# Optimization experiments

Hardware: AMD Instinct MI355X
Metric: run time of the kernel (lower is better)

The kernel has to match this reference:

```python
import jax, jax.numpy as jnp
import numpy as np


def setup_inputs() -> dict:
    key = jax.random.key(0)
    k1, k2 = jax.random.split(key)
    B, C, H, W = 4, 64, 256, 256
    x = jax.random.normal(k1, (B, C, H, W), dtype=jnp.float32)
    perspective = jax.random.uniform(k2, (B, 1, H, W), dtype=jnp.float32)
    alpha = jnp.ones((1,), dtype=jnp.float32) * 3.0   # sigma scale
    beta = jnp.ones((1,), dtype=jnp.float32)          # sigmoid slope
    gamma = jnp.zeros((1,), dtype=jnp.float32)        # sigmoid shift
    return {"x": x, "perspective": perspective, "alpha": alpha,
            "beta": beta, "gamma": gamma, "kernel_size": 7}


def reference(x, perspective, alpha, beta, gamma, kernel_size):
    K = int(kernel_size)
    pad = K // 2
    B, C, H, W = x.shape
    # AdaptiveSigmoid sigma map, clamped like the torch module
    sigma = jnp.maximum(alpha * jax.nn.sigmoid(beta * perspective + gamma), 1e-4)  # [B,1,H,W]
    inv2s2 = 1.0 / (2.0 * sigma * sigma)                                           # [B,1,H,W]
    # squared distance of each kernel tap from center (static)
    offs = np.arange(K) - pad
    d2 = (offs[:, None] ** 2 + offs[None, :] ** 2).reshape(-1).astype(np.float32)  # [K*K]
    # per-pixel, per-tap Gaussian weights, normalized over taps
    w = jnp.exp(-d2[:, None, None, None, None] * inv2s2[None])  # [K*K,B,1,H,W]
    w = w / jnp.sum(w, axis=0)
    xp = jnp.pad(x, ((0, 0), (0, 0), (pad, pad), (pad, pad)))
    out = jnp.zeros_like(x)
    k = 0
    for i in range(K):            # fixed small K*K loop (49 taps), jit-friendly
        for j in range(K):
            out = out + w[k] * xp[:, :, i:i + H, j:j + W]
            k += 1
    return out
```

## Files before the change

kernel.cpp:

```cpp
#include <hip/hip_runtime.h>

#define NB 4
#define NC 64
#define NH 256
#define NW 256
#define TH 32
#define LR 38
#define LSTR 264
#define NCHUNK 66
#define NCHUNKS_TOT (LR * NCHUNK)
#define BUF_BYTES (NCHUNKS_TOT * 16)
#define CH_PER 4

__device__ float g_zero[16] __attribute__((aligned(64)));

static __device__ __forceinline__ void async16(const void* g, void* l) {
    __builtin_amdgcn_global_load_lds(
        (const __attribute__((address_space(1))) void*)g,
        (__attribute__((address_space(3))) void*)l, 16, 0, 0);
}

__global__ __launch_bounds__(256, 2)
void adaptive_gauss7(const float* __restrict__ x,
                     const float* __restrict__ persp,
                     const float* __restrict__ alpha_p,
                     const float* __restrict__ beta_p,
                     const float* __restrict__ gamma_p,
                     float* __restrict__ out)
{
    __shared__ char xs_raw[2 * BUF_BYTES];

    const int tid  = threadIdx.x;
    const int lane = tid & 63;
    const int wv   = tid >> 6;
    const int c0   = blockIdx.x * CH_PER;
    const int h0   = blockIdx.y * TH;
    const int b    = blockIdx.z;
    const int colbase = lane * 4;
    const int rbase   = wv * 8;

    const float alpha = alpha_p[0];
    const float beta  = beta_p[0];
    const float gamma = gamma_p[0];

    float4 pv4[8];
    {
        const float* pp = persp + (size_t)b * NH * NW;
        #pragma unroll
        for (int r = 0; r < 8; ++r)
            pv4[r] = *(const float4*)(pp + (size_t)(h0 + rbase + r) * NW + colbase);
    }

    int offs[10];
    #pragma unroll
    for (int it = 0; it < 10; ++it) {
        const int q  = it * 256 + tid;
        const int r  = q / NCHUNK;
        const int cb = (q - r * NCHUNK) * 16 - 16;
        const int gr = h0 - 3 + r;
        const bool valid = ((unsigned)gr < NH) && ((unsigned)cb < NW * 4);
        offs[it] = valid ? (gr * (NW * 4) + cb) : -1;
    }

    const char* xbase = (const char*)x + (size_t)(b * NC + c0) * NH * NW * 4;

    auto stage = [&](int bufsel, int ci) {
        const char* xc = xbase + (size_t)ci * NH * NW * 4;
        char* lb = xs_raw + bufsel * BUF_BYTES + wv * 1024;
        #pragma unroll
        for (int it = 0; it < 10; ++it) {
            if (it < 9 || (it * 256 + tid) < NCHUNKS_TOT) {
                const char* g = (offs[it] >= 0) ? (xc + offs[it]) : (const char*)g_zero;
                async16(g, lb + it * 4096);
            }
        }
    };

    stage(0, 0);

    float gw[8][4];
    #pragma unroll
    for (int r = 0; r < 8; ++r) {
        const float pv[4] = {pv4[r].x, pv4[r].y, pv4[r].z, pv4[r].w};
        #pragma unroll
        for (int k = 0; k < 4; ++k) {
            const float z  = fmaf(beta, pv[k], gamma);
            const float sg = __builtin_amdgcn_rcpf(1.0f + __expf(-z));
            const float sigma = fmaxf(alpha * sg, 1e-4f);
            const float t  = 0.5f * __builtin_amdgcn_rcpf(sigma * sigma);
            gw[r][k] = __expf(-t);
        }
    }

    __syncthreads();

    for (int ci = 0; ci < CH_PER; ++ci) {
        if (ci + 1 < CH_PER)
            stage((ci + 1) & 1, ci + 1);

        const float* xs = (const float*)(xs_raw + (ci & 1) * BUF_BYTES);

        float win[7][12];
        #pragma unroll
        for (int i = 0; i < 7; ++i) {
            const float* src = &xs[(rbase + i) * LSTR + colbase];
            const float4 a0 = *(const float4*)(src);
            const float4 a1 = *(const float4*)(src + 4);
            const float4 a2 = *(const float4*)(src + 8);
            win[i][0] = a0.x; win[i][1] = a0.y; win[i][2]  = a0.z; win[i][3]  = a0.w;
            win[i][4] = a1.x; win[i][5] = a1.y; win[i][6]  = a1.z; win[i][7]  = a1.w;
            win[i][8] = a2.x; win[i][9] = a2.y; win[i][10] = a2.z; win[i][11] = a2.w;
        }

        float* outp = out + (size_t)(b * NC + c0 + ci) * NH * NW
                          + (size_t)(h0 + rbase) * NW + colbase;

        #pragma unroll
        for (int orow = 0; orow < 8; ++orow) {
            if (orow > 0) {
                const int wi = (orow + 6) % 7;
                const float* src = &xs[(rbase + orow + 6) * LSTR + colbase];
                const float4 a0 = *(const float4*)(src);
                const float4 a1 = *(const float4*)(src + 4);
                const float4 a2 = *(const float4*)(src + 8);
                win[wi][0] = a0.x; win[wi][1] = a0.y; win[wi][2]  = a0.z; win[wi][3]  = a0.w;
                win[wi][4] = a1.x; win[wi][5] = a1.y; win[wi][6]  = a1.z; win[wi][7]  = a1.w;
                win[wi][8] = a2.x; win[wi][9] = a2.y; win[wi][10] = a2.z; win[wi][11] = a2.w;
            }
            float res[4];
            #pragma unroll
            for (int k = 0; k < 4; ++k) {
                const float g  = gw[orow][k];
                const float g2 = g * g;
                const float p4 = g2 * g2;
                const float p9 = p4 * p4 * g;
                const float S  = fmaf(2.0f, (g + p4) + p9, 1.0f);
                const float inv  = __builtin_amdgcn_rcpf(S);
                const float inv2 = inv * inv;
                float rs[7];
                #pragma unroll
                for (int j = 0; j < 7; ++j) {
                    const int wr = (orow + j) % 7;
                    rs[j] = fmaf(p9, win[wr][k+1] + win[wr][k+7],
                            fmaf(p4, win[wr][k+2] + win[wr][k+6],
                            fmaf(g,  win[wr][k+3] + win[wr][k+5],
                                     win[wr][k+4])));
                }
                const float acc = fmaf(p9, rs[0] + rs[6],
                                  fmaf(p4, rs[1] + rs[5],
                                  fmaf(g,  rs[2] + rs[4],
                                           rs[3])));
                res[k] = acc * inv2;
            }
            *(float4*)(outp + (size_t)orow * NW) =
                make_float4(res[0], res[1], res[2], res[3]);
        }

        __syncthreads();
    }
}

extern "C" void kernel_launch(void* const* d_in, const int* in_sizes, int n_in,
                              void* d_out, int out_size, void* d_ws, size_t ws_size,
                              hipStream_t stream) {
    const float* x     = (const float*)d_in[0];
    const float* persp = (const float*)d_in[1];
    const float* alpha = (const float*)d_in[2];
    const float* beta  = (const float*)d_in[3];
    const float* gamma = (const float*)d_in[4];
    float* outp        = (float*)d_out;
    dim3 grid(NC / CH_PER, NH / TH, NB);
    adaptive_gauss7<<<grid, dim3(256), 0, stream>>>(x, persp, alpha, beta, gamma, outp);
}
```

Measured before the change: 152.5 us.

## Shrink row tile and channels per block, single-buffer LDS, drop register window

Halves the row tile to 16 and channels per block to 2, and replaces the double-buffered LDS stage with a single buffer that is refilled between channels under barriers. The sliding 7-row register window is replaced by re-reading all 7 LDS rows for every output row. Smaller LDS and register use are meant to raise occupancy and produce more blocks. The cost is more halo traffic per block (22 rows loaded for 16 outputs), serialized loads with no overlap, and more LDS reads.

```diff
diff --git a/kernel.cpp b/kernel.cpp
--- a/kernel.cpp
+++ b/kernel.cpp
@@ -4,13 +4,13 @@
 #define NC 64
 #define NH 256
 #define NW 256
-#define TH 32
-#define LR 38
+#define TH 16
+#define LR 22
 #define LSTR 264
 #define NCHUNK 66
 #define NCHUNKS_TOT (LR * NCHUNK)
 #define BUF_BYTES (NCHUNKS_TOT * 16)
-#define CH_PER 4
+#define CH_PER 2
 
 __device__ float g_zero[16] __attribute__((aligned(64)));
 
@@ -28,7 +28,7 @@
                      const float* __restrict__ gamma_p,
                      float* __restrict__ out)
 {
-    __shared__ char xs_raw[2 * BUF_BYTES];
+    __shared__ char xs_raw[BUF_BYTES];
 
     const int tid  = threadIdx.x;
     const int lane = tid & 63;
@@ -37,23 +37,15 @@
     const int h0   = blockIdx.y * TH;
     const int b    = blockIdx.z;
     const int colbase = lane * 4;
-    const int rbase   = wv * 8;
+    const int rbase   = wv * 4;
 
     const float alpha = alpha_p[0];
     const float beta  = beta_p[0];
     const float gamma = gamma_p[0];
 
-    float4 pv4[8];
-    {
-        const float* pp = persp + (size_t)b * NH * NW;
-        #pragma unroll
-        for (int r = 0; r < 8; ++r)
-            pv4[r] = *(const float4*)(pp + (size_t)(h0 + rbase + r) * NW + colbase);
-    }
-
-    int offs[10];
+    int offs[6];
     #pragma unroll
-    for (int it = 0; it < 10; ++it) {
+    for (int it = 0; it < 6; ++it) {
         const int q  = it * 256 + tid;
         const int r  = q / NCHUNK;
         const int cb = (q - r * NCHUNK) * 16 - 16;
@@ -64,99 +56,96 @@
 
     const char* xbase = (const char*)x + (size_t)(b * NC + c0) * NH * NW * 4;
 
-    auto stage = [&](int bufsel, int ci) {
+    auto stage = [&](int ci) {
         const char* xc = xbase + (size_t)ci * NH * NW * 4;
-        char* lb = xs_raw + bufsel * BUF_BYTES + wv * 1024;
+        char* lb = xs_raw + wv * 1024;
         #pragma unroll
-        for (int it = 0; it < 10; ++it) {
-            if (it < 9 || (it * 256 + tid) < NCHUNKS_TOT) {
+        for (int it = 0; it < 6; ++it) {
+            if (it < 5 || tid < (NCHUNKS_TOT - 5 * 256)) {
                 const char* g = (offs[it] >= 0) ? (xc + offs[it]) : (const char*)g_zero;
                 async16(g, lb + it * 4096);
             }
         }
     };
 
-    stage(0, 0);
+    stage(0);
 
-    float gw[8][4];
-    #pragma unroll
-    for (int r = 0; r < 8; ++r) {
-        const float pv[4] = {pv4[r].x, pv4[r].y, pv4[r].z, pv4[r].w};
+    float gwv[4][4];
+    {
+        const float* pp = persp + (size_t)b * NH * NW;
         #pragma unroll
-        for (int k = 0; k < 4; ++k) {
-            const float z  = fmaf(beta, pv[k], gamma);
-            const float sg = __builtin_amdgcn_rcpf(1.0f + __expf(-z));
-            const float sigma = fmaxf(alpha * sg, 1e-4f);
-            const float t  = 0.5f * __builtin_amdgcn_rcpf(sigma * sigma);
-            gw[r][k] = __expf(-t);
+        for (int r = 0; r < 4; ++r) {
+            const float4 p4v = *(const float4*)(pp + (size_t)(h0 + rbase + r) * NW + colbase);
+            const float pv[4] = {p4v.x, p4v.y, p4v.z, p4v.w};
+            #pragma unroll
+            for (int k = 0; k < 4; ++k) {
+                const float z  = fmaf(beta, pv[k], gamma);
+                const float sg = __builtin_amdgcn_rcpf(1.0f + __expf(-z));
+                const float sigma = fmaxf(alpha * sg, 1e-4f);
+                const float t  = 0.5f * __builtin_amdgcn_rcpf(sigma * sigma);
+                gwv[r][k] = __expf(-t);
+            }
         }
     }
 
     __syncthreads();
 
+    #pragma unroll
     for (int ci = 0; ci < CH_PER; ++ci) {
-        if (ci + 1 < CH_PER)
-            stage((ci + 1) & 1, ci + 1);
-
-        const float* xs = (const float*)(xs_raw + (ci & 1) * BUF_BYTES);
-
-        float win[7][12];
-        #pragma unroll
-        for (int i = 0; i < 7; ++i) {
-            const float* src = &xs[(rbase + i) * LSTR + colbase];
-            const float4 a0 = *(const float4*)(src);
-            const float4 a1 = *(const float4*)(src + 4);
-            const float4 a2 = *(const float4*)(src + 8);
-            win[i][0] = a0.x; win[i][1] = a0.y; win[i][2]  = a0.z; win[i][3]  = a0.w;
-            win[i][4] = a1.x; win[i][5] = a1.y; win[i][6]  = a1.z; win[i][7]  = a1.w;
-            win[i][8] = a2.x; win[i][9] = a2.y; win[i][10] = a2.z; win[i][11] = a2.w;
-        }
-
+        const float* xs = (const float*)xs_raw;
         float* outp = out + (size_t)(b * NC + c0 + ci) * NH * NW
                           + (size_t)(h0 + rbase) * NW + colbase;
 
         #pragma unroll
-        for (int orow = 0; orow < 8; ++orow) {
-            if (orow > 0) {
-                const int wi = (orow + 6) % 7;
-                const float* src = &xs[(rbase + orow + 6) * LSTR + colbase];
-                const float4 a0 = *(const float4*)(src);
-                const float4 a1 = *(const float4*)(src + 4);
-                const float4 a2 = *(const float4*)(src + 8);
-                win[wi][0] = a0.x; win[wi][1] = a0.y; win[wi][2]  = a0.z; win[wi][3]  = a0.w;
-                win[wi][4] = a1.x; win[wi][5] = a1.y; win[wi][6]  = a1.z; win[wi][7]  = a1.w;
-                win[wi][8] = a2.x; win[wi][9] = a2.y; win[wi][10] = a2.z; win[wi][11] = a2.w;
-            }
-            float res[4];
+        for (int orow = 0; orow < 4; ++orow) {
+            const float* src = &xs[(rbase + orow) * LSTR + colbase];
+
+            float G[4], P4[4], P9[4], INV2[4];
             #pragma unroll
             for (int k = 0; k < 4; ++k) {
-                const float g  = gw[orow][k];
+                const float g  = gwv[orow][k];
                 const float g2 = g * g;
-                const float p4 = g2 * g2;
-                const float p9 = p4 * p4 * g;
-                const float S  = fmaf(2.0f, (g + p4) + p9, 1.0f);
-                const float inv  = __builtin_amdgcn_rcpf(S);
-                const float inv2 = inv * inv;
-                float rs[7];
+                G[k]  = g;
+                P4[k] = g2 * g2;
+                P9[k] = P4[k] * P4[k] * g;
+                const float S = fmaf(2.0f, (g + P4[k]) + P9[k], 1.0f);
+                const float inv = __builtin_amdgcn_rcpf(S);
+                INV2[k] = inv * inv;
+            }
+
+            float acc[4] = {0.f, 0.f, 0.f, 0.f};
+            #pragma unroll
+            for (int j = 0; j < 7; ++j) {
+                const float* rp = src + j * LSTR;
+                const float4 a0 = *(const float4*)(rp);
+                const float4 a1 = *(const float4*)(rp + 4);
+                const float4 a2 = *(const float4*)(rp + 8);
+                const float w[12] = {a0.x, a0.y, a0.z, a0.w,
+                                     a1.x, a1.y, a1.z, a1.w,
+                                     a2.x, a2.y, a2.z, a2.w};
                 #pragma unroll
-                for (int j = 0; j < 7; ++j) {
-                    const int wr = (orow + j) % 7;
-                    rs[j] = fmaf(p9, win[wr][k+1] + win[wr][k+7],
-                            fmaf(p4, win[wr][k+2] + win[wr][k+6],
-                            fmaf(g,  win[wr][k+3] + win[wr][k+5],
-                                     win[wr][k+4])));
+                for (int k = 0; k < 4; ++k) {
+                    const float rs =
+                        fmaf(P9[k], w[k+1] + w[k+7],
+                        fmaf(P4[k], w[k+2] + w[k+6],
+                        fmaf(G[k],  w[k+3] + w[k+5],
+                                    w[k+4])));
+                    const float vw = (j == 0 || j == 6) ? P9[k]
+                                   : (j == 1 || j == 5) ? P4[k]
+                                   : (j == 2 || j == 4) ? G[k] : 1.0f;
+                    acc[k] = fmaf(vw, rs, acc[k]);
                 }
-                const float acc = fmaf(p9, rs[0] + rs[6],
-                                  fmaf(p4, rs[1] + rs[5],
-                                  fmaf(g,  rs[2] + rs[4],
-                                           rs[3])));
-                res[k] = acc * inv2;
             }
             *(float4*)(outp + (size_t)orow * NW) =
-                make_float4(res[0], res[1], res[2], res[3]);
+                make_float4(acc[0] * INV2[0], acc[1] * INV2[1],
+                            acc[2] * INV2[2], acc[3] * INV2[3]);
         }
 
-        __syncthreads();
+        if (ci + 1 < CH_PER) {
+            __syncthreads();
+            stage(ci + 1);
+            __syncthreads();
+        }
     }
 }
 
```

Measured after the change: 178.1 us. +16.8%, slower.
